# Kernel optimization log

Measured on AMD Instinct MI355X. Metric: run time of the kernel, lower is better.

Reference implementation:

```python
import jax, jax.numpy as jnp
import numpy as np

D = 768      # hidden_size
H = 12       # num_head
HD = D // H  # head_dim
LN_EPS = 1e-5


def setup_inputs() -> dict:
    key = jax.random.key(0)
    ks = jax.random.split(key, 9)
    N, S = 4, 2048
    s = 0.02
    return {
        "hidden_state": jax.random.normal(ks[0], (N, S, D), dtype=jnp.float32),
        "key_padding_mask": jax.random.randint(ks[1], (N, S), 0, 2, dtype=jnp.int64),
        "Wq": jax.random.normal(ks[2], (D, D), dtype=jnp.float32) * s,
        "Wk": jax.random.normal(ks[3], (D, D), dtype=jnp.float32) * s,
        "Wv": jax.random.normal(ks[4], (D, D), dtype=jnp.float32) * s,
        "Wo": jax.random.normal(ks[5], (D, D), dtype=jnp.float32) * s,
        "W1": jax.random.normal(ks[6], (4 * D, D), dtype=jnp.float32) * s,
        "W2": jax.random.normal(ks[7], (D, 4 * D), dtype=jnp.float32) * s,
        "ln_g": jnp.ones((D,), dtype=jnp.float32),
        "ln_b": jnp.zeros((D,), dtype=jnp.float32),
    }


def _layernorm(x, g, b):
    mu = jnp.mean(x, axis=-1, keepdims=True)
    var = jnp.mean(jnp.square(x - mu), axis=-1, keepdims=True)
    return (x - mu) * jax.lax.rsqrt(var + LN_EPS) * g + b


def reference(hidden_state, key_padding_mask, Wq, Wk, Wv, Wo, W1, W2, ln_g, ln_b):
    x = hidden_state
    N, S, _ = x.shape
    # Note: original module projects K and V from `query` (self-attention).
    def proj(W):
        return (x @ W.T).reshape(N, S, H, HD).transpose(0, 2, 1, 3)  # [N,H,S,HD]
    Q, K, V = proj(Wq), proj(Wk), proj(Wv)
    scores = jnp.einsum("bhqd,bhkd->bhqk", Q, K)  # [N,H,S,S]
    # int mask: 0 marks padding positions -> masked with -inf
    pad = (key_padding_mask == 0)[:, None, None, :]  # [N,1,1,S]
    scores = jnp.where(pad, -jnp.inf, scores)
    attn = jax.nn.softmax(scores / np.sqrt(HD), axis=-1)
    ctx = jnp.einsum("bhqk,bhkd->bhqd", attn, V)
    ctx = ctx.transpose(0, 2, 1, 3).reshape(N, S, D)
    mha = ctx @ Wo.T
    # residual + LayerNorm (same LN params used twice, as in the original)
    n1 = _layernorm(x + mha, ln_g, ln_b)
    # FFN with exact GELU (torch nn.GELU default)
    f = jax.nn.gelu(n1 @ W1.T, approximate=False) @ W2.T
    return _layernorm(n1 + f, ln_g, ln_b)
```

## Files before the change

kernel.cpp:

```cpp
#include <hip/hip_runtime.h>
#include <math.h>

typedef unsigned short u16;
typedef unsigned int u32;
typedef __bf16 bf16x8 __attribute__((ext_vector_type(8)));
typedef float f32x4 __attribute__((ext_vector_type(4)));
typedef u32 u32x4 __attribute__((ext_vector_type(4)));

#define NB 4
#define SS 2048
#define DD 768
#define HH 12
#define HD 64
#define ROWS (NB*SS)

__device__ __forceinline__ u16 f2bf(float f) {
    union { float f; unsigned u; } v; v.f = f;
    unsigned r = v.u + 0x7fffu + ((v.u >> 16) & 1u);
    return (u16)(r >> 16);
}
__device__ __forceinline__ u32 fas(float f) { union { float f; u32 u; } v; v.f = f; return v.u; }

__device__ __forceinline__ void gl_lds16(const void* g, void* l) {
    __builtin_amdgcn_global_load_lds((__attribute__((address_space(1))) void*)(g),
                                     (__attribute__((address_space(3))) void*)(l),
                                     16, 0, 0);
}

__global__ __launch_bounds__(256) void prep_kernel(
        const float* __restrict__ X, const float* __restrict__ Wq,
        const float* __restrict__ Wk, const float* __restrict__ Wv,
        const float* __restrict__ Wo, const float* __restrict__ W1,
        const float* __restrict__ W2, const int* __restrict__ mask,
        u16* __restrict__ Xb, u16* __restrict__ Wqkvb, u16* __restrict__ Wob,
        u16* __restrict__ W1b, u16* __restrict__ W2b,
        int* __restrict__ cidx, int* __restrict__ cnt) {
    const int blk = blockIdx.x, tid = threadIdx.x;
    const float* src; u16* dst; int idx;
    if (blk < 6144)       { src = X;  dst = Xb;               idx = blk * 1024 + tid * 4; }
    else if (blk < 6720)  { src = Wq; dst = Wqkvb;            idx = (blk - 6144) * 1024 + tid * 4; }
    else if (blk < 7296)  { src = Wk; dst = Wqkvb + DD * DD;  idx = (blk - 6720) * 1024 + tid * 4; }
    else if (blk < 7872)  { src = Wv; dst = Wqkvb + 2*DD*DD;  idx = (blk - 7296) * 1024 + tid * 4; }
    else if (blk < 8448)  { src = Wo; dst = Wob;              idx = (blk - 7872) * 1024 + tid * 4; }
    else if (blk < 10752) { src = W1; dst = W1b;              idx = (blk - 8448) * 1024 + tid * 4; }
    else if (blk < 13056) { src = W2; dst = W2b;              idx = (blk - 10752) * 1024 + tid * 4; }
    else {
        const int b = blk - 13056;
        const int lane = tid & 63, wave = tid >> 6;
        const int base = b * SS + tid * 8;
        int4 m0 = *(const int4*)&mask[base];
        int4 m1 = *(const int4*)&mask[base + 4];
        int v[8] = { m0.x != 0, m0.y != 0, m0.z != 0, m0.w != 0,
                     m1.x != 0, m1.y != 0, m1.z != 0, m1.w != 0 };
        int own = 0;
#pragma unroll
        for (int i = 0; i < 8; ++i) own += v[i];
        int inc = own;
#pragma unroll
        for (int o = 1; o < 64; o <<= 1) {
            int n = __shfl_up(inc, o);
            if (lane >= o) inc += n;
        }
        __shared__ int wsum[4];
        if (lane == 63) wsum[wave] = inc;
        __syncthreads();
        int wbase = 0;
#pragma unroll
        for (int w = 0; w < 4; ++w) wbase += (w < wave) ? wsum[w] : 0;
        int pos = wbase + inc - own;
        int o8[8];
#pragma unroll
        for (int i = 0; i < 8; ++i) { o8[i] = v[i] ? pos : -1; pos += v[i]; }
        *(int4*)&cidx[base]     = make_int4(o8[0], o8[1], o8[2], o8[3]);
        *(int4*)&cidx[base + 4] = make_int4(o8[4], o8[5], o8[6], o8[7]);
        if (tid == 255) cnt[b] = wbase + inc;
        return;
    }
    float4 v = *(const float4*)&src[idx];
    ushort4 o;
    o.x = f2bf(v.x); o.y = f2bf(v.y); o.z = f2bf(v.z); o.w = f2bf(v.w);
    *(ushort4*)&dst[idx] = o;
}

template <int EPI, int BN, int BK, int BM>
__global__ __launch_bounds__(BM * 2) void gemm_bt(const u16* __restrict__ A,
                                                  const u16* __restrict__ B,
                                                  int M, int N, int K,
                                                  void* __restrict__ out,
                                                  const void* __restrict__ aux,
                                                  u16* __restrict__ Qb,
                                                  u16* __restrict__ Kb,
                                                  u16* __restrict__ Vb,
                                                  const int* __restrict__ cidx) {
    constexpr int NH = BK / 64;
    constexpr int NT = BM * 2;
    constexpr int MPX = (ROWS / BM) / 8;
    __shared__ __align__(16) u16 lA[NH][BM * 64];
    __shared__ __align__(16) u16 lB[NH][BN * 64];
    constexpr int MI = (BN == 128) ? 4 : 2;
    const int tid = threadIdx.x;
    const int lane = tid & 63, wave = tid >> 6;
    const int quad = lane >> 4, lc = lane & 15;
    const int xcd = blockIdx.x & 7, loc = blockIdx.x >> 3;
    const int mb = xcd * MPX + (loc % MPX), nb = loc / MPX;
    const int m0 = mb * BM, n0 = nb * BN;
    const int wrow = (BN == 128) ? (wave >> 1) * 64 : wave * 32;
    const int wcol = (BN == 128) ? (wave & 1) * 64 : 0;
    const int swz = lc & 7;

    f32x4 acc[MI][4] = {};

    for (int kb = 0; kb < K; kb += BK) {
        __syncthreads();
#pragma unroll
        for (int h = 0; h < NH; ++h) {
#pragma unroll
            for (int p0 = 0; p0 < BM * 8; p0 += NT) {
                int p = p0 + tid, row = p >> 3, cl = (p & 7) ^ (row & 7);
                gl_lds16(A + (size_t)(m0 + row) * K + kb + h * 64 + cl * 8,
                         &lA[h][(size_t)(p0 + wave * 64) * 8]);
            }
#pragma unroll
            for (int p0 = 0; p0 < BN * 8; p0 += NT) {
                int p = p0 + tid, row = p >> 3, cl = (p & 7) ^ (row & 7);
                gl_lds16(B + (size_t)(n0 + row) * K + kb + h * 64 + cl * 8,
                         &lB[h][(size_t)(p0 + wave * 64) * 8]);
            }
        }
        __syncthreads();
#pragma unroll
        for (int h = 0; h < NH; ++h)
#pragma unroll
            for (int k2 = 0; k2 < 2; ++k2) {
                bf16x8 af[MI], bfr[4];
#pragma unroll
                for (int t = 0; t < MI; ++t)
                    af[t] = *(const bf16x8*)&lA[h][(wrow + t * 16 + lc) * 64 + ((quad + k2 * 4) ^ swz) * 8];
#pragma unroll
                for (int t = 0; t < 4; ++t)
                    bfr[t] = *(const bf16x8*)&lB[h][(wcol + t * 16 + lc) * 64 + ((quad + k2 * 4) ^ swz) * 8];
#pragma unroll
                for (int mi = 0; mi < MI; ++mi)
#pragma unroll
                    for (int ni = 0; ni < 4; ++ni)
                        acc[mi][ni] = __builtin_amdgcn_mfma_f32_16x16x32_bf16(af[mi], bfr[ni],
                                                                             acc[mi][ni], 0, 0, 0);
            }
    }

#pragma unroll
    for (int mi = 0; mi < MI; ++mi) {
        int csa[4];
        if constexpr (EPI == 0) {
            int mbase = m0 + wrow + mi * 16 + quad * 4;
            int4 cs4 = *(const int4*)&cidx[(mbase >> 11) * SS + (mbase & 2047)];
            csa[0] = cs4.x; csa[1] = cs4.y; csa[2] = cs4.z; csa[3] = cs4.w;
        }
#pragma unroll
        for (int r = 0; r < 4; ++r) {
            int m = m0 + wrow + mi * 16 + quad * 4 + r;
#pragma unroll
            for (int ni = 0; ni < 4; ++ni) {
                int n = n0 + wcol + ni * 16 + lc;
                float v = acc[mi][ni][r];
                if constexpr (EPI == 0) {
                    int b = m >> 11, s = m & 2047;
                    int which = n / DD, rem = n - which * DD;
                    int h = rem >> 6, d = rem & 63;
                    u16* dst = which == 0 ? Qb : (which == 1 ? Kb : Vb);
                    int sidx = which == 0 ? s : csa[r];
                    if (sidx >= 0)
                        dst[((((size_t)b * HH + h) * SS + sidx) << 6) + d] = f2bf(v);
                } else if constexpr (EPI == 1) {
                    float u = v * fmaf(v * v, 0.035677408f, 0.7978845608f);
                    float e = __builtin_amdgcn_exp2f(u * 2.885390082f);
                    float g = v - v * __builtin_amdgcn_rcpf(e + 1.0f);
                    ((u16*)out)[(size_t)m * N + n] = f2bf(g);
                } else if constexpr (EPI == 2) {
                    ((float*)out)[(size_t)m * N + n] =
                        v + ((const float*)aux)[(size_t)m * N + n];
                } else {
                    ((float*)out)[(size_t)m * N + n] =
                        v + (float)(((const __bf16*)aux)[(size_t)m * N + n]);
                }
            }
        }
    }
}

__global__ __launch_bounds__(256) void transpose_v(const u16* __restrict__ V,
                                                   u16* __restrict__ Vt,
                                                   const int* __restrict__ cnt) {
    __shared__ u16 t[32][33];
    int bh = blockIdx.z;
    int c = cnt[bh / HH];
    int cr = (c + 63) & ~63;
    int s0 = blockIdx.x * 32, d0 = blockIdx.y * 32;
    if (s0 >= cr) return;
    const u16* vb = V + (size_t)bh * SS * HD;
    u16* vtb = Vt + (size_t)bh * HD * SS;
    int tx = threadIdx.x & 31, ty = threadIdx.x >> 5;
#pragma unroll
    for (int i = 0; i < 32; i += 8) {
        int s = s0 + ty + i;
        t[ty + i][tx] = (s < c) ? vb[(size_t)s * HD + d0 + tx] : (u16)0;
    }
    __syncthreads();
#pragma unroll
    for (int i = 0; i < 32; i += 8) vtb[(size_t)(d0 + ty + i) * SS + s0 + tx] = t[tx][ty + i];
}

__global__ __launch_bounds__(256, 3) void attn_kernel(const u16* __restrict__ Q,
                                                      const u16* __restrict__ K,
                                                      const u16* __restrict__ Vt,
                                                      const int* __restrict__ cntg,
                                                      u16* __restrict__ Ctx) {
    __shared__ __align__(16) u16 lK[2][4096];
    __shared__ __align__(16) u16 lV[2][4096];
    const int tid = threadIdx.x, lane = tid & 63, wave = tid >> 6;
    const int quad = lane >> 4, lc = lane & 15;
    const int bh = blockIdx.x % (NB * HH);
    const int b = bh / HH, h = bh - b * HH;
    const int q0 = (blockIdx.x / (NB * HH)) * 128;
    const u16* Qg = Q + ((size_t)bh * SS + q0 + wave * 32) * HD;
    const u16* Kg = K + (size_t)bh * SS * HD;
    const u16* Vg = Vt + (size_t)bh * HD * SS;
    const int sw = lc & 7;
    const int cnt = cntg[b];
    const int nt = (cnt + 63) >> 6;

    const int srow = tid >> 3, scl = (tid & 7) ^ (srow & 7);
    const int srow2 = (256 + tid) >> 3, scl2 = (tid & 7) ^ (srow2 & 7);

    auto stage = [&](int bi, int j0) {
        gl_lds16(Kg + (size_t)(j0 + srow) * HD + scl * 8,   &lK[bi][(size_t)(wave * 64) * 8]);
        gl_lds16(Kg + (size_t)(j0 + srow2) * HD + scl2 * 8, &lK[bi][(size_t)(256 + wave * 64) * 8]);
        gl_lds16(Vg + (size_t)srow * SS + j0 + scl * 8,     &lV[bi][(size_t)(wave * 64) * 8]);
        gl_lds16(Vg + (size_t)srow2 * SS + j0 + scl2 * 8,   &lV[bi][(size_t)(256 + wave * 64) * 8]);
    };

    bf16x8 qf[2][2];
#pragma unroll
    for (int mi = 0; mi < 2; ++mi)
#pragma unroll
        for (int k2 = 0; k2 < 2; ++k2)
            qf[mi][k2] = *(const bf16x8*)(Qg + (size_t)(mi * 16 + lc) * HD + k2 * 32 + quad * 8);

    bf16x8 onesf;
#pragma unroll
    for (int i = 0; i < 8; ++i) onesf[i] = (__bf16)1.0f;

    f32x4 oacc[2][4] = {};
    f32x4 lsum[2] = {};

    stage(0, 0);
    for (int t = 0; t < nt; ++t) {
        const int cur = t & 1;
        if (t < nt - 1) {
            stage(cur ^ 1, (t + 1) * 64);
            __builtin_amdgcn_sched_barrier(0);
            asm volatile("s_waitcnt vmcnt(4)" ::: "memory");
        } else {
            __builtin_amdgcn_sched_barrier(0);
            asm volatile("s_waitcnt vmcnt(0)" ::: "memory");
        }
        __builtin_amdgcn_sched_barrier(0);
        __builtin_amdgcn_s_barrier();
        __builtin_amdgcn_sched_barrier(0);

        const u16* bK = &lK[cur][0];
        const u16* bV = &lV[cur][0];

        f32x4 sacc[2][4] = {};
        __builtin_amdgcn_s_setprio(1);
#pragma unroll
        for (int k2 = 0; k2 < 2; ++k2) {
            bf16x8 kf[4];
#pragma unroll
            for (int ni = 0; ni < 4; ++ni)
                kf[ni] = *(const bf16x8*)&bK[(ni * 16 + lc) * 64 + ((quad + k2 * 4) ^ sw) * 8];
#pragma unroll
            for (int ni = 0; ni < 4; ++ni) {
                sacc[0][ni] = __builtin_amdgcn_mfma_f32_16x16x32_bf16(kf[ni], qf[0][k2], sacc[0][ni], 0, 0, 0);
                sacc[1][ni] = __builtin_amdgcn_mfma_f32_16x16x32_bf16(kf[ni], qf[1][k2], sacc[1][ni], 0, 0, 0);
            }
        }
        __builtin_amdgcn_s_setprio(0);

        const int kb_ = cnt - t * 64;
        const bool part = kb_ < 64;
        u32 pa[2][4], pb[2][4];
#pragma unroll
        for (int ni = 0; ni < 4; ++ni) {
#pragma unroll
            for (int mi = 0; mi < 2; ++mi) {
#pragma unroll
                for (int r = 0; r < 4; ++r) {
                    float e = __builtin_amdgcn_exp2f(sacc[mi][ni][r] * 0.180336880f);
                    if (part) e = (ni * 16 + quad * 4 + r < kb_) ? e : 0.0f;
                    sacc[mi][ni][r] = e;
                }
                pa[mi][ni] = __builtin_amdgcn_perm(fas(sacc[mi][ni][1]), fas(sacc[mi][ni][0]), 0x07060302);
                pb[mi][ni] = __builtin_amdgcn_perm(fas(sacc[mi][ni][3]), fas(sacc[mi][ni][2]), 0x07060302);
            }
        }

        bf16x8 pf[2][2];
#pragma unroll
        for (int mi = 0; mi < 2; ++mi)
#pragma unroll
            for (int k2 = 0; k2 < 2; ++k2) {
                u32 xa = pa[mi][2 * k2], ya = pa[mi][2 * k2 + 1];
                u32 xb = pb[mi][2 * k2], yb = pb[mi][2 * k2 + 1];
                asm("v_permlane32_swap_b32 %0, %1" : "+v"(xa), "+v"(ya));
                asm("v_permlane16_swap_b32 %0, %1" : "+v"(xa), "+v"(ya));
                asm("v_permlane32_swap_b32 %0, %1" : "+v"(xb), "+v"(yb));
                asm("v_permlane16_swap_b32 %0, %1" : "+v"(xb), "+v"(yb));
                u32x4 pw = { xa, xb, ya, yb };
                pf[mi][k2] = __builtin_bit_cast(bf16x8, pw);
            }

        __builtin_amdgcn_s_setprio(1);
#pragma unroll
        for (int k2 = 0; k2 < 2; ++k2) {
            lsum[0] = __builtin_amdgcn_mfma_f32_16x16x32_bf16(pf[0][k2], onesf, lsum[0], 0, 0, 0);
            lsum[1] = __builtin_amdgcn_mfma_f32_16x16x32_bf16(pf[1][k2], onesf, lsum[1], 0, 0, 0);
#pragma unroll
            for (int ni = 0; ni < 4; ++ni) {
                bf16x8 vf = *(const bf16x8*)&bV[(ni * 16 + lc) * 64 + ((quad + k2 * 4) ^ sw) * 8];
                oacc[0][ni] = __builtin_amdgcn_mfma_f32_16x16x32_bf16(pf[0][k2], vf, oacc[0][ni], 0, 0, 0);
                oacc[1][ni] = __builtin_amdgcn_mfma_f32_16x16x32_bf16(pf[1][k2], vf, oacc[1][ni], 0, 0, 0);
            }
        }
        __builtin_amdgcn_s_setprio(0);

        __builtin_amdgcn_sched_barrier(0);
        __builtin_amdgcn_s_barrier();
    }

#pragma unroll
    for (int mi = 0; mi < 2; ++mi)
#pragma unroll
        for (int r = 0; r < 4; ++r) {
            float inv = 1.0f / lsum[mi][r];
            int s = q0 + wave * 32 + mi * 16 + quad * 4 + r;
            size_t base = ((size_t)(b * SS + s)) * DD + h * HD;
#pragma unroll
            for (int ni = 0; ni < 4; ++ni)
                Ctx[base + ni * 16 + lc] = f2bf(oacc[mi][ni][r] * inv);
        }
}

__global__ __launch_bounds__(256) void ln_kernel(const float* __restrict__ in,
                                                 const float* __restrict__ g,
                                                 const float* __restrict__ bb,
                                                 u16* __restrict__ out_bf,
                                                 float* __restrict__ out_f) {
    const int row = blockIdx.x, tid = threadIdx.x;
    const float* x = in + (size_t)row * DD;
    float v0 = x[tid], v1 = x[tid + 256], v2 = x[tid + 512];
    float s = v0 + v1 + v2;
    float q = v0 * v0 + v1 * v1 + v2 * v2;
#pragma unroll
    for (int o = 1; o < 64; o <<= 1) {
        s += __shfl_xor(s, o);
        q += __shfl_xor(q, o);
    }
    __shared__ float rs[4], rq[4];
    int wave = tid >> 6;
    if ((tid & 63) == 0) { rs[wave] = s; rq[wave] = q; }
    __syncthreads();
    s = rs[0] + rs[1] + rs[2] + rs[3];
    q = rq[0] + rq[1] + rq[2] + rq[3];
    float mu = s * (1.0f / DD);
    float var = q * (1.0f / DD) - mu * mu;
    float rstd = rsqrtf(var + 1e-5f);
#pragma unroll
    for (int j = 0; j < 3; ++j) {
        int col = tid + j * 256;
        float v = (j == 0 ? v0 : (j == 1 ? v1 : v2));
        float y = (v - mu) * rstd * g[col] + bb[col];
        if (out_bf) out_bf[(size_t)row * DD + col] = f2bf(y);
        if (out_f) out_f[(size_t)row * DD + col] = y;
    }
}

extern "C" void kernel_launch(void* const* d_in, const int* in_sizes, int n_in,
                              void* d_out, int out_size, void* d_ws, size_t ws_size,
                              hipStream_t stream) {
    const float* X    = (const float*)d_in[0];
    const int*   mask = (const int*)d_in[1];
    const float* Wq   = (const float*)d_in[2];
    const float* Wk   = (const float*)d_in[3];
    const float* Wv   = (const float*)d_in[4];
    const float* Wo   = (const float*)d_in[5];
    const float* W1   = (const float*)d_in[6];
    const float* W2   = (const float*)d_in[7];
    const float* ln_g = (const float*)d_in[8];
    const float* ln_b = (const float*)d_in[9];
    float* out = (float*)d_out;

    char* ws = (char*)d_ws;
    size_t off = 0;
    auto alloc = [&](size_t bytes) {
        void* p = ws + off;
        off += (bytes + 255) & ~(size_t)255;
        return p;
    };
    u16*   Xbf   = (u16*)alloc((size_t)ROWS * DD * 2);
    u16*   Wqkvb = (u16*)alloc((size_t)3 * DD * DD * 2);
    u16*   Wob   = (u16*)alloc((size_t)DD * DD * 2);
    u16*   W1b   = (u16*)alloc((size_t)4 * DD * DD * 2);
    u16*   W2b   = (u16*)alloc((size_t)4 * DD * DD * 2);
    int*   cidx  = (int*)alloc((size_t)NB * SS * 4);
    int*   cnt   = (int*)alloc(256);
    u16*   Qb    = (u16*)alloc((size_t)ROWS * DD * 2);
    u16*   Kb    = (u16*)alloc((size_t)ROWS * DD * 2);
    u16*   Vb    = (u16*)alloc((size_t)ROWS * DD * 2);
    u16*   Vtb   = (u16*)alloc((size_t)ROWS * DD * 2);
    float* resid = (float*)alloc((size_t)ROWS * DD * 4);
    u16*   n1b   = (u16*)alloc((size_t)ROWS * DD * 2);
    u16*   Gb    = Qb;
    u16*   Ctxb  = Xbf;
    float* h2    = resid;

    prep_kernel<<<dim3(13056 + NB), dim3(256), 0, stream>>>(
        X, Wq, Wk, Wv, Wo, W1, W2, mask,
        Xbf, Wqkvb, Wob, W1b, W2b, cidx, cnt);

    gemm_bt<0, 128, 64, 128><<<dim3((3 * DD / 128) * (ROWS / 128)), dim3(256), 0, stream>>>(
        Xbf, Wqkvb, ROWS, 3 * DD, DD, nullptr, nullptr, Qb, Kb, Vb, cidx);

    transpose_v<<<dim3(SS / 32, HD / 32, NB * HH), dim3(256), 0, stream>>>(Vb, Vtb, cnt);

    attn_kernel<<<dim3((SS / 128) * (NB * HH)), dim3(256), 0, stream>>>(
        Qb, Kb, Vtb, cnt, Ctxb);

    gemm_bt<2, 64, 128, 128><<<dim3((DD / 64) * (ROWS / 128)), dim3(256), 0, stream>>>(
        Ctxb, Wob, ROWS, DD, DD, resid, X, nullptr, nullptr, nullptr, nullptr);

    ln_kernel<<<dim3(ROWS), dim3(256), 0, stream>>>(resid, ln_g, ln_b, n1b, nullptr);

    gemm_bt<1, 128, 64, 256><<<dim3((4 * DD / 128) * (ROWS / 256)), dim3(512), 0, stream>>>(
        n1b, W1b, ROWS, 4 * DD, DD, Gb, nullptr, nullptr, nullptr, nullptr, nullptr);

    gemm_bt<3, 64, 128, 128><<<dim3((DD / 64) * (ROWS / 128)), dim3(256), 0, stream>>>(
        Gb, W2b, ROWS, DD, 4 * DD, h2, n1b, nullptr, nullptr, nullptr, nullptr);

    ln_kernel<<<dim3(ROWS), dim3(256), 0, stream>>>(h2, ln_g, ln_b, nullptr, out);
}
```

Measured before the change: 333.8 us.

## Gather unmasked rows for K/V projection and skip padded row tiles

The QKV GEMM is split into a Q-only GEMM and a K/V GEMM. The mask prep kernel now writes a compacted list of unmasked row indices. The K/V GEMM gathers A rows through that list and exits early for tiles past the valid count, so K and V are not computed for padded keys (about half the rows with a random mask). This adds a second launch and indirect row loads. The final tile's rows past the count read zero-initialised indices, and their outputs land in slots attention ignores.

```diff
diff --git a/kernel.cpp b/kernel.cpp
--- a/kernel.cpp
+++ b/kernel.cpp
@@ -52,6 +52,8 @@
         int4 m1 = *(const int4*)&mask[base + 4];
         int v[8] = { m0.x != 0, m0.y != 0, m0.z != 0, m0.w != 0,
                      m1.x != 0, m1.y != 0, m1.z != 0, m1.w != 0 };
+        *(int4*)&cidx[base]     = make_int4(0, 0, 0, 0);
+        *(int4*)&cidx[base + 4] = make_int4(0, 0, 0, 0);
         int own = 0;
 #pragma unroll
         for (int i = 0; i < 8; ++i) own += v[i];
@@ -68,11 +70,9 @@
 #pragma unroll
         for (int w = 0; w < 4; ++w) wbase += (w < wave) ? wsum[w] : 0;
         int pos = wbase + inc - own;
-        int o8[8];
-#pragma unroll
-        for (int i = 0; i < 8; ++i) { o8[i] = v[i] ? pos : -1; pos += v[i]; }
-        *(int4*)&cidx[base]     = make_int4(o8[0], o8[1], o8[2], o8[3]);
-        *(int4*)&cidx[base + 4] = make_int4(o8[4], o8[5], o8[6], o8[7]);
+#pragma unroll
+        for (int i = 0; i < 8; ++i)
+            if (v[i]) { cidx[b * SS + pos] = tid * 8 + i; ++pos; }
         if (tid == 255) cnt[b] = wbase + inc;
         return;
     }
@@ -95,6 +95,7 @@
     constexpr int NH = BK / 64;
     constexpr int NT = BM * 2;
     constexpr int MPX = (ROWS / BM) / 8;
+    constexpr int AR = BM * 8 / NT;
     __shared__ __align__(16) u16 lA[NH][BM * 64];
     __shared__ __align__(16) u16 lB[NH][BN * 64];
     constexpr int MI = (BN == 128) ? 4 : 2;
@@ -108,6 +109,21 @@
     const int wcol = (BN == 128) ? (wave & 1) * 64 : 0;
     const int swz = lc & 7;
 
+    const int b_ = m0 >> 11;
+    if constexpr (EPI == 4) {
+        if ((m0 & 2047) >= ((const int*)aux)[b_]) return;
+    }
+
+    int grow[AR];
+#pragma unroll
+    for (int i = 0; i < AR; ++i) {
+        int p = i * NT + tid, row = p >> 3;
+        if constexpr (EPI == 4)
+            grow[i] = (b_ << 11) + cidx[m0 + row];
+        else
+            grow[i] = m0 + row;
+    }
+
     f32x4 acc[MI][4] = {};
 
     for (int kb = 0; kb < K; kb += BK) {
@@ -117,7 +133,7 @@
 #pragma unroll
             for (int p0 = 0; p0 < BM * 8; p0 += NT) {
                 int p = p0 + tid, row = p >> 3, cl = (p & 7) ^ (row & 7);
-                gl_lds16(A + (size_t)(m0 + row) * K + kb + h * 64 + cl * 8,
+                gl_lds16(A + (size_t)grow[p0 / NT] * K + kb + h * 64 + cl * 8,
                          &lA[h][(size_t)(p0 + wave * 64) * 8]);
             }
 #pragma unroll
@@ -150,12 +166,6 @@
 
 #pragma unroll
     for (int mi = 0; mi < MI; ++mi) {
-        int csa[4];
-        if constexpr (EPI == 0) {
-            int mbase = m0 + wrow + mi * 16 + quad * 4;
-            int4 cs4 = *(const int4*)&cidx[(mbase >> 11) * SS + (mbase & 2047)];
-            csa[0] = cs4.x; csa[1] = cs4.y; csa[2] = cs4.z; csa[3] = cs4.w;
-        }
 #pragma unroll
         for (int r = 0; r < 4; ++r) {
             int m = m0 + wrow + mi * 16 + quad * 4 + r;
@@ -165,12 +175,14 @@
                 float v = acc[mi][ni][r];
                 if constexpr (EPI == 0) {
                     int b = m >> 11, s = m & 2047;
-                    int which = n / DD, rem = n - which * DD;
+                    int h = n >> 6, d = n & 63;
+                    Qb[((((size_t)b * HH + h) * SS + s) << 6) + d] = f2bf(v);
+                } else if constexpr (EPI == 4) {
+                    int b = m >> 11, local = m & 2047;
+                    int which = (n >= DD), rem = n - which * DD;
                     int h = rem >> 6, d = rem & 63;
-                    u16* dst = which == 0 ? Qb : (which == 1 ? Kb : Vb);
-                    int sidx = which == 0 ? s : csa[r];
-                    if (sidx >= 0)
-                        dst[((((size_t)b * HH + h) * SS + sidx) << 6) + d] = f2bf(v);
+                    u16* dst = which ? Vb : Kb;
+                    dst[((((size_t)b * HH + h) * SS + local) << 6) + d] = f2bf(v);
                 } else if constexpr (EPI == 1) {
                     float u = v * fmaf(v * v, 0.035677408f, 0.7978845608f);
                     float e = __builtin_amdgcn_exp2f(u * 2.885390082f);
@@ -428,8 +440,11 @@
         X, Wq, Wk, Wv, Wo, W1, W2, mask,
         Xbf, Wqkvb, Wob, W1b, W2b, cidx, cnt);
 
-    gemm_bt<0, 128, 64, 128><<<dim3((3 * DD / 128) * (ROWS / 128)), dim3(256), 0, stream>>>(
-        Xbf, Wqkvb, ROWS, 3 * DD, DD, nullptr, nullptr, Qb, Kb, Vb, cidx);
+    gemm_bt<0, 128, 64, 128><<<dim3((DD / 128) * (ROWS / 128)), dim3(256), 0, stream>>>(
+        Xbf, Wqkvb, ROWS, DD, DD, nullptr, nullptr, Qb, nullptr, nullptr, nullptr);
+
+    gemm_bt<4, 128, 64, 128><<<dim3((2 * DD / 128) * (ROWS / 128)), dim3(256), 0, stream>>>(
+        Xbf, Wqkvb + DD * DD, ROWS, 2 * DD, DD, nullptr, cnt, nullptr, Kb, Vb, cidx);
 
     transpose_v<<<dim3(SS / 32, HD / 32, NB * HH), dim3(256), 0, stream>>>(Vb, Vtb, cnt);
 
```

Result: slower. 342.2 us (+2.5%).

## Double-buffer LDS tiles with async prefetch in BN=64 GEMMs

Applied to the files above, without the earlier changes.

Adds a PIPE template mode to the bf16 GEMM that double-buffers LDS tiles with BK=64. It issues the next tile's global-to-LDS loads before computing the current one and waits with an explicit vmcnt count. The Wo and W2 projection GEMMs switch to this mode (BK shrinks from 128 to 64), while the QKV and W1 GEMMs keep the old single-stage loop. The aim is to hide global load latency behind MFMA work. The cost is two barriers per 64-wide K step and a hand-coded vmcnt literal that relies on exactly six loads per tile.

```diff
diff --git a/kernel.cpp b/kernel.cpp
--- a/kernel.cpp
+++ b/kernel.cpp
@@ -82,7 +82,7 @@
     *(ushort4*)&dst[idx] = o;
 }
 
-template <int EPI, int BN, int BK, int BM>
+template <int EPI, int BN, int BK, int BM, int PIPE>
 __global__ __launch_bounds__(BM * 2) void gemm_bt(const u16* __restrict__ A,
                                                   const u16* __restrict__ B,
                                                   int M, int N, int K,
@@ -93,10 +93,12 @@
                                                   u16* __restrict__ Vb,
                                                   const int* __restrict__ cidx) {
     constexpr int NH = BK / 64;
+    constexpr int NBUF = PIPE ? 2 : NH;
     constexpr int NT = BM * 2;
     constexpr int MPX = (ROWS / BM) / 8;
-    __shared__ __align__(16) u16 lA[NH][BM * 64];
-    __shared__ __align__(16) u16 lB[NH][BN * 64];
+    static_assert(!PIPE || NH == 1, "PIPE=1 requires BK=64");
+    __shared__ __align__(16) u16 lA[NBUF][BM * 64];
+    __shared__ __align__(16) u16 lB[NBUF][BN * 64];
     constexpr int MI = (BN == 128) ? 4 : 2;
     const int tid = threadIdx.x;
     const int lane = tid & 63, wave = tid >> 6;
@@ -110,42 +112,71 @@
 
     f32x4 acc[MI][4] = {};
 
-    for (int kb = 0; kb < K; kb += BK) {
-        __syncthreads();
-#pragma unroll
-        for (int h = 0; h < NH; ++h) {
-#pragma unroll
-            for (int p0 = 0; p0 < BM * 8; p0 += NT) {
-                int p = p0 + tid, row = p >> 3, cl = (p & 7) ^ (row & 7);
-                gl_lds16(A + (size_t)(m0 + row) * K + kb + h * 64 + cl * 8,
-                         &lA[h][(size_t)(p0 + wave * 64) * 8]);
-            }
-#pragma unroll
-            for (int p0 = 0; p0 < BN * 8; p0 += NT) {
-                int p = p0 + tid, row = p >> 3, cl = (p & 7) ^ (row & 7);
-                gl_lds16(B + (size_t)(n0 + row) * K + kb + h * 64 + cl * 8,
-                         &lB[h][(size_t)(p0 + wave * 64) * 8]);
-            }
-        }
-        __syncthreads();
-#pragma unroll
-        for (int h = 0; h < NH; ++h)
-#pragma unroll
-            for (int k2 = 0; k2 < 2; ++k2) {
-                bf16x8 af[MI], bfr[4];
-#pragma unroll
-                for (int t = 0; t < MI; ++t)
-                    af[t] = *(const bf16x8*)&lA[h][(wrow + t * 16 + lc) * 64 + ((quad + k2 * 4) ^ swz) * 8];
-#pragma unroll
-                for (int t = 0; t < 4; ++t)
-                    bfr[t] = *(const bf16x8*)&lB[h][(wcol + t * 16 + lc) * 64 + ((quad + k2 * 4) ^ swz) * 8];
-#pragma unroll
-                for (int mi = 0; mi < MI; ++mi)
-#pragma unroll
-                    for (int ni = 0; ni < 4; ++ni)
-                        acc[mi][ni] = __builtin_amdgcn_mfma_f32_16x16x32_bf16(af[mi], bfr[ni],
-                                                                             acc[mi][ni], 0, 0, 0);
-            }
+    auto stage1 = [&](int bi, int kb) {
+#pragma unroll
+        for (int p0 = 0; p0 < BM * 8; p0 += NT) {
+            int p = p0 + tid, row = p >> 3, cl = (p & 7) ^ (row & 7);
+            gl_lds16(A + (size_t)(m0 + row) * K + kb + cl * 8,
+                     &lA[bi][(size_t)(p0 + wave * 64) * 8]);
+        }
+#pragma unroll
+        for (int p0 = 0; p0 < BN * 8; p0 += NT) {
+            int p = p0 + tid, row = p >> 3, cl = (p & 7) ^ (row & 7);
+            gl_lds16(B + (size_t)(n0 + row) * K + kb + cl * 8,
+                     &lB[bi][(size_t)(p0 + wave * 64) * 8]);
+        }
+    };
+
+    auto compute64 = [&](int bi) {
+#pragma unroll
+        for (int k2 = 0; k2 < 2; ++k2) {
+            bf16x8 af[MI], bfr[4];
+#pragma unroll
+            for (int t = 0; t < MI; ++t)
+                af[t] = *(const bf16x8*)&lA[bi][(wrow + t * 16 + lc) * 64 + ((quad + k2 * 4) ^ swz) * 8];
+#pragma unroll
+            for (int t = 0; t < 4; ++t)
+                bfr[t] = *(const bf16x8*)&lB[bi][(wcol + t * 16 + lc) * 64 + ((quad + k2 * 4) ^ swz) * 8];
+#pragma unroll
+            for (int mi = 0; mi < MI; ++mi)
+#pragma unroll
+                for (int ni = 0; ni < 4; ++ni)
+                    acc[mi][ni] = __builtin_amdgcn_mfma_f32_16x16x32_bf16(af[mi], bfr[ni],
+                                                                         acc[mi][ni], 0, 0, 0);
+        }
+    };
+
+    if constexpr (PIPE == 0) {
+        for (int kb = 0; kb < K; kb += BK) {
+            __syncthreads();
+#pragma unroll
+            for (int h = 0; h < NH; ++h) stage1(h, kb + h * 64);
+            __syncthreads();
+#pragma unroll
+            for (int h = 0; h < NH; ++h) compute64(h);
+        }
+    } else {
+        constexpr int NLD = (BM * 8 + BN * 8) / NT;
+        static_assert(NLD == 6, "vmcnt literal assumes 6 loads per tile");
+        const int KT = K >> 6;
+        stage1(0, 0);
+        for (int t = 0; t < KT; ++t) {
+            const int cur = t & 1;
+            if (t < KT - 1) {
+                stage1(cur ^ 1, (t + 1) << 6);
+                __builtin_amdgcn_sched_barrier(0);
+                asm volatile("s_waitcnt vmcnt(6)" ::: "memory");
+            } else {
+                __builtin_amdgcn_sched_barrier(0);
+                asm volatile("s_waitcnt vmcnt(0)" ::: "memory");
+            }
+            __builtin_amdgcn_sched_barrier(0);
+            __builtin_amdgcn_s_barrier();
+            __builtin_amdgcn_sched_barrier(0);
+            compute64(cur);
+            __builtin_amdgcn_sched_barrier(0);
+            __builtin_amdgcn_s_barrier();
+        }
     }
 
 #pragma unroll
@@ -428,7 +459,7 @@
         X, Wq, Wk, Wv, Wo, W1, W2, mask,
         Xbf, Wqkvb, Wob, W1b, W2b, cidx, cnt);
 
-    gemm_bt<0, 128, 64, 128><<<dim3((3 * DD / 128) * (ROWS / 128)), dim3(256), 0, stream>>>(
+    gemm_bt<0, 128, 64, 128, 0><<<dim3((3 * DD / 128) * (ROWS / 128)), dim3(256), 0, stream>>>(
         Xbf, Wqkvb, ROWS, 3 * DD, DD, nullptr, nullptr, Qb, Kb, Vb, cidx);
 
     transpose_v<<<dim3(SS / 32, HD / 32, NB * HH), dim3(256), 0, stream>>>(Vb, Vtb, cnt);
@@ -436,15 +467,15 @@
     attn_kernel<<<dim3((SS / 128) * (NB * HH)), dim3(256), 0, stream>>>(
         Qb, Kb, Vtb, cnt, Ctxb);
 
-    gemm_bt<2, 64, 128, 128><<<dim3((DD / 64) * (ROWS / 128)), dim3(256), 0, stream>>>(
+    gemm_bt<2, 64, 64, 128, 1><<<dim3((DD / 64) * (ROWS / 128)), dim3(256), 0, stream>>>(
         Ctxb, Wob, ROWS, DD, DD, resid, X, nullptr, nullptr, nullptr, nullptr);
 
     ln_kernel<<<dim3(ROWS), dim3(256), 0, stream>>>(resid, ln_g, ln_b, n1b, nullptr);
 
-    gemm_bt<1, 128, 64, 256><<<dim3((4 * DD / 128) * (ROWS / 256)), dim3(512), 0, stream>>>(
+    gemm_bt<1, 128, 64, 256, 0><<<dim3((4 * DD / 128) * (ROWS / 256)), dim3(512), 0, stream>>>(
         n1b, W1b, ROWS, 4 * DD, DD, Gb, nullptr, nullptr, nullptr, nullptr, nullptr);
 
-    gemm_bt<3, 64, 128, 128><<<dim3((DD / 64) * (ROWS / 128)), dim3(256), 0, stream>>>(
+    gemm_bt<3, 64, 64, 128, 1><<<dim3((DD / 64) * (ROWS / 128)), dim3(256), 0, stream>>>(
         Gb, W2b, ROWS, DD, 4 * DD, h2, n1b, nullptr, nullptr, nullptr, nullptr);
 
     ln_kernel<<<dim3(ROWS), dim3(256), 0, stream>>>(h2, ln_g, ln_b, nullptr, out);
```

After: 340.9 us. +2.1%, slower.
